# Performance work log

Measured on AMD Instinct MI355X. Metric: run time of the kernel, lower is better.

The kernel has to match this reference:

```python
import jax, jax.numpy as jnp
import numpy as np

VOCAB = 267735
CUTOFFS = [20000, 40000, 200000, VOCAB]  # self.cutoffs (incl. vocab)
SHORTLIST = 20000
N_CLUSTERS = 3


def setup_inputs() -> dict:
    key = jax.random.key(0)
    ks = jax.random.split(key, 16)
    s = 0.02  # init scale as in reset_parameters / linear_weight_init
    return {
        "x": jax.random.normal(ks[0], (1024, 1024), jnp.float32),
        "target": jax.random.randint(ks[1], (1024,), 0, VOCAB, jnp.int64),
        "W0": s * jax.random.normal(ks[2], (20000, 1024), jnp.float32),
        "b0": jnp.zeros((20000,), jnp.float32),
        "W1": s * jax.random.normal(ks[3], (20000, 256), jnp.float32),
        "b1": jnp.zeros((20000,), jnp.float32),
        "W2": s * jax.random.normal(ks[4], (160000, 64), jnp.float32),
        "b2": jnp.zeros((160000,), jnp.float32),
        "W3": s * jax.random.normal(ks[5], (67735, 16), jnp.float32),
        "b3": jnp.zeros((67735,), jnp.float32),
        "cluster_weight": s * jax.random.normal(ks[6], (3, 1024), jnp.float32),
        "cluster_bias": jnp.zeros((3,), jnp.float32),
        "P0": s * jax.random.normal(ks[7], (1024, 1024), jnp.float32),
        "P1": s * jax.random.normal(ks[8], (1024, 256), jnp.float32),
        "P2": s * jax.random.normal(ks[9], (1024, 64), jnp.float32),
        "P3": s * jax.random.normal(ks[10], (1024, 16), jnp.float32),
    }


def _logits(x, P, W, b):
    # F.linear(hidden, proj.t()) == x @ proj ; then F.linear(proj_hid, W, b)
    return (x @ P) @ W.T + b


def reference(x, target, W0, b0, W1, b1, W2, b2, W3, b3,
              cluster_weight, cluster_bias, P0, P1, P2, P3):
    N = x.shape[0]
    # head: shortlist + cluster logits
    head_w = jnp.concatenate([W0, cluster_weight], axis=0)  # [20003, 1024]
    head_b = jnp.concatenate([b0, cluster_bias], axis=0)
    head_logp = jax.nn.log_softmax(_logits(x, P0, head_w, head_b), axis=-1)

    # remap targets falling in tail clusters to their cluster token in the head
    # cluster idx -> head index SHORTLIST + N_CLUSTERS - 1 - idx
    head_idx = target
    for idx in range(N_CLUSTERS):
        l, r = CUTOFFS[idx], CUTOFFS[idx + 1]
        in_c = (target >= l) & (target < r)
        head_idx = jnp.where(in_c, SHORTLIST + N_CLUSTERS - 1 - idx, head_idx)

    nll = -jnp.take_along_axis(head_logp, head_idx[:, None], axis=1)[:, 0]

    # tail clusters: dense masked cross-entropy (same math as gather/scatter
    # version: each token contributes only its own cluster's CE)
    tails = [(W1, b1, P1), (W2, b2, P2), (W3, b3, P3)]
    for idx, (W, b, P) in enumerate(tails):
        l, r = CUTOFFS[idx], CUTOFFS[idx + 1]
        mask = (target >= l) & (target < r)
        t = jnp.clip(target - l, 0, r - l - 1)
        logp = jax.nn.log_softmax(_logits(x, P, W, b), axis=-1)  # [N, r-l]
        ce = -jnp.take_along_axis(logp, t[:, None], axis=1)[:, 0]
        nll = nll + jnp.where(mask, ce, jnp.zeros_like(ce))
    return nll
```

## Files before the change

### kernel.cpp

```cpp
#include <hip/hip_runtime.h>
#include <hip/hip_bf16.h>
#include <math.h>


typedef __attribute__((ext_vector_type(4))) float f32x4;
typedef __attribute__((ext_vector_type(8))) short bf16x8;
typedef __attribute__((ext_vector_type(8))) unsigned short ushort8;

#define NEG_INF (-INFINITY)

static __device__ __forceinline__ unsigned short f2b(float f) {
  unsigned u = __builtin_bit_cast(unsigned, f);
  u += 0x7fffu + ((u >> 16) & 1u);
  return (unsigned short)(u >> 16);
}
static __device__ __forceinline__ f32x4 zero4() { f32x4 z = {0.f,0.f,0.f,0.f}; return z; }
static __device__ __forceinline__ ushort8 zero8() { ushort8 z = {0,0,0,0,0,0,0,0}; return z; }

__global__ __launch_bounds__(256, 3)
void gemm_lse(const unsigned short* __restrict__ A, const float* __restrict__ B,
              const float* __restrict__ bias, int V, int K, int T,
              float* __restrict__ parts)
{
  __shared__ unsigned short As[128 * 40];
  __shared__ unsigned short Bs[128 * 40];
  __shared__ float red[2][128];

  const int t = threadIdx.x;
  const int rowBase = blockIdx.y * 128;
  const int strip = blockIdx.x;
  const int KS = (K + 31) >> 5;

  const int ar = t >> 1, ak = (t & 1) << 4;
  const int br = t >> 1, bk = (t & 1) << 4;
  const size_t arow = (size_t)(rowBase + ar) * K;

  ushort8 aSb[2]; f32x4 bS[4];
  auto LOADB = [&](int tile, int k0) {
    size_t row = (size_t)(strip * T + tile) * 128 + br;
    bool v = row < (size_t)V;
    const float* bp = B + row * (size_t)K;
    #pragma unroll
    for (int i = 0; i < 4; ++i) {
      int k = k0 + bk + i * 4;
      bS[i] = (v && (k + 4 <= K)) ? *(const f32x4*)(bp + k) : zero4();
    }
  };
  auto LOADA = [&](int k0) {
    #pragma unroll
    for (int i = 0; i < 2; ++i) {
      int k = k0 + ak + i * 8;
      aSb[i] = (k + 8 <= K) ? *(const ushort8*)(A + arow + k) : zero8();
    }
  };
  auto STORE = [&]() {
    *(ushort8*)&As[ar * 40 + ak]     = aSb[0];
    *(ushort8*)&As[ar * 40 + ak + 8] = aSb[1];
    ushort8 p0, p1;
    #pragma unroll
    for (int j = 0; j < 4; ++j) {
      p0[j] = f2b(bS[0][j]); p0[j + 4] = f2b(bS[1][j]);
      p1[j] = f2b(bS[2][j]); p1[j + 4] = f2b(bS[3][j]);
    }
    *(ushort8*)&Bs[br * 40 + bk]     = p0;
    *(ushort8*)&Bs[br * 40 + bk + 8] = p1;
  };

  const int lane = t & 63, w = t >> 6;
  const int wr = w >> 1, wc = w & 1;
  const int g = lane >> 4, fr = lane & 15;

  float S[4][4];
  #pragma unroll
  for (int m = 0; m < 4; ++m)
    #pragma unroll
    for (int r = 0; r < 4; ++r) S[m][r] = 0.f;
  f32x4 acc[4][4];
  #pragma unroll
  for (int m = 0; m < 4; ++m)
    #pragma unroll
    for (int n = 0; n < 4; ++n) acc[m][n] = zero4();

  float bcol[4];
  LOADB(0, 0); LOADA(0);
  int tile = 0, ks = 0;
  const int total = T * KS;
  for (int step = 0; step < total; ++step) {
    __syncthreads();
    STORE();
    __syncthreads();
    if (ks == 0) {
      #pragma unroll
      for (int n = 0; n < 4; ++n) {
        int col = (strip * T + tile) * 128 + wc * 64 + n * 16 + fr;
        bcol[n] = (col < V) ? bias[col] : NEG_INF;
      }
    }
    const bool last = (ks == KS - 1);
    int nt = tile, nk = ks + 1;
    if (nk == KS) { nk = 0; nt++; }
    if (nt < T) { LOADB(nt, nk * 32); LOADA(nk * 32); }
    bf16x8 af[4], bfr[4];
    #pragma unroll
    for (int m = 0; m < 4; ++m)
      af[m] = *(const bf16x8*)&As[(wr * 64 + m * 16 + fr) * 40 + g * 8];
    #pragma unroll
    for (int n = 0; n < 4; ++n)
      bfr[n] = *(const bf16x8*)&Bs[(wc * 64 + n * 16 + fr) * 40 + g * 8];
    #pragma unroll
    for (int m = 0; m < 4; ++m)
      #pragma unroll
      for (int n = 0; n < 4; ++n)
        acc[m][n] = __builtin_amdgcn_mfma_f32_16x16x32_bf16(af[m], bfr[n], acc[m][n], 0, 0, 0);
    if (last) {
      #pragma unroll
      for (int m = 0; m < 4; ++m)
        #pragma unroll
        for (int n = 0; n < 4; ++n)
          #pragma unroll
          for (int r = 0; r < 4; ++r)
            S[m][r] += __expf(acc[m][n][r] + bcol[n]);
      #pragma unroll
      for (int m = 0; m < 4; ++m)
        #pragma unroll
        for (int n = 0; n < 4; ++n) acc[m][n] = zero4();
    }
    tile = nt; ks = nk;
  }

  #pragma unroll
  for (int off = 1; off <= 8; off <<= 1)
    #pragma unroll
    for (int m = 0; m < 4; ++m)
      #pragma unroll
      for (int r = 0; r < 4; ++r) S[m][r] += __shfl_xor(S[m][r], off, 64);
  if (fr == 0) {
    #pragma unroll
    for (int m = 0; m < 4; ++m)
      #pragma unroll
      for (int r = 0; r < 4; ++r) red[wc][wr * 64 + m * 16 + g * 4 + r] = S[m][r];
  }
  __syncthreads();
  if (t < 128) parts[(size_t)strip * 1024 + rowBase + t] = red[0][t] + red[1][t];
}

__global__ __launch_bounds__(256, 3)
void gemm_proj(const float* __restrict__ A, const unsigned short* __restrict__ B,
               int V, int K,
               float* __restrict__ Cf, unsigned short* __restrict__ Cb)
{
  __shared__ unsigned short As[128 * 40];
  __shared__ unsigned short Bs[128 * 40];

  const int t = threadIdx.x;
  const int rowBase = blockIdx.y * 128;
  const int colBase = blockIdx.x * 128;

  const int ar = t >> 1, ak = (t & 1) << 4;
  const int br = t >> 1, bk = (t & 1) << 4;
  const bool bval = (colBase + br) < V;
  const size_t arow = (size_t)(rowBase + ar) * K;
  const size_t brow = (size_t)(colBase + br) * K;

  f32x4 aS[4]; ushort8 bSb[2];
  auto LOAD = [&](int k0) {
    #pragma unroll
    for (int i = 0; i < 4; ++i) aS[i] = *(const f32x4*)(A + arow + k0 + ak + i * 4);
    bSb[0] = bval ? *(const ushort8*)(B + brow + k0 + bk)     : zero8();
    bSb[1] = bval ? *(const ushort8*)(B + brow + k0 + bk + 8) : zero8();
  };
  auto STORE = [&]() {
    ushort8 p0, p1;
    #pragma unroll
    for (int j = 0; j < 4; ++j) {
      p0[j] = f2b(aS[0][j]); p0[j + 4] = f2b(aS[1][j]);
      p1[j] = f2b(aS[2][j]); p1[j + 4] = f2b(aS[3][j]);
    }
    *(ushort8*)&As[ar * 40 + ak]     = p0;
    *(ushort8*)&As[ar * 40 + ak + 8] = p1;
    *(ushort8*)&Bs[br * 40 + bk]     = bSb[0];
    *(ushort8*)&Bs[br * 40 + bk + 8] = bSb[1];
  };

  const int lane = t & 63, w = t >> 6;
  const int wr = w >> 1, wc = w & 1;
  const int g = lane >> 4, fr = lane & 15;

  f32x4 acc[4][4];
  #pragma unroll
  for (int m = 0; m < 4; ++m)
    #pragma unroll
    for (int n = 0; n < 4; ++n) acc[m][n] = zero4();

  LOAD(0);
  for (int k0 = 0; k0 < K; k0 += 32) {
    __syncthreads();
    STORE();
    __syncthreads();
    if (k0 + 32 < K) LOAD(k0 + 32);
    bf16x8 af[4], bfr[4];
    #pragma unroll
    for (int m = 0; m < 4; ++m)
      af[m] = *(const bf16x8*)&As[(wr * 64 + m * 16 + fr) * 40 + g * 8];
    #pragma unroll
    for (int n = 0; n < 4; ++n)
      bfr[n] = *(const bf16x8*)&Bs[(wc * 64 + n * 16 + fr) * 40 + g * 8];
    #pragma unroll
    for (int m = 0; m < 4; ++m)
      #pragma unroll
      for (int n = 0; n < 4; ++n)
        acc[m][n] = __builtin_amdgcn_mfma_f32_16x16x32_bf16(af[m], bfr[n], acc[m][n], 0, 0, 0);
  }

  #pragma unroll
  for (int m = 0; m < 4; ++m) {
    int row = rowBase + wr * 64 + m * 16 + g * 4;
    #pragma unroll
    for (int n = 0; n < 4; ++n) {
      int col = colBase + wc * 64 + n * 16 + fr;
      if (col < V) {
        #pragma unroll
        for (int r = 0; r < 4; ++r) {
          float v = acc[m][n][r];
          Cf[(size_t)(row + r) * V + col] = v;
          Cb[(size_t)(row + r) * V + col] = f2b(v);
        }
      }
    }
  }
}

__global__ void transpose_k(const float* __restrict__ P, unsigned short* __restrict__ PT, int N)
{
  __shared__ float tile[32][33];
  int tx = threadIdx.x, ty = threadIdx.y;
  int n0 = blockIdx.x * 32, k0 = blockIdx.y * 32;
  #pragma unroll
  for (int j = 0; j < 32; j += 8) {
    int n = n0 + tx;
    tile[ty + j][tx] = (n < N) ? P[(size_t)(k0 + ty + j) * N + n] : 0.f;
  }
  __syncthreads();
  #pragma unroll
  for (int j = 0; j < 32; j += 8) {
    int n = n0 + ty + j;
    if (n < N) PT[(size_t)n * 1024 + (k0 + tx)] = f2b(tile[tx][ty + j]);
  }
}

__global__ void cluster_logits_k(const float* __restrict__ H0,
                                 const float* __restrict__ CW,
                                 const float* __restrict__ cb,
                                 float* __restrict__ clog)
{
  int wid = (blockIdx.x * blockDim.x + threadIdx.x) >> 6;
  int lane = threadIdx.x & 63;
  if (wid >= 1024) return;
  float s0 = 0.f, s1 = 0.f, s2 = 0.f;
  for (int k = lane * 4; k < 1024; k += 256) {
    f32x4 h  = *(const f32x4*)&H0[(size_t)wid * 1024 + k];
    f32x4 w0 = *(const f32x4*)&CW[k];
    f32x4 w1 = *(const f32x4*)&CW[1024 + k];
    f32x4 w2 = *(const f32x4*)&CW[2048 + k];
    #pragma unroll
    for (int j = 0; j < 4; ++j) { s0 += h[j]*w0[j]; s1 += h[j]*w1[j]; s2 += h[j]*w2[j]; }
  }
  #pragma unroll
  for (int off = 1; off <= 32; off <<= 1) {
    s0 += __shfl_xor(s0, off, 64);
    s1 += __shfl_xor(s1, off, 64);
    s2 += __shfl_xor(s2, off, 64);
  }
  if (lane == 0) {
    clog[wid * 3 + 0] = s0 + cb[0];
    clog[wid * 3 + 1] = s1 + cb[1];
    clog[wid * 3 + 2] = s2 + cb[2];
  }
}

__global__ void head_target_k(const float* __restrict__ H0,
                              const float* __restrict__ W0,
                              const float* __restrict__ b0,
                              const float* __restrict__ clog,
                              const int* __restrict__ target,
                              float* __restrict__ headT)
{
  int wid = (blockIdx.x * blockDim.x + threadIdx.x) >> 6;
  int lane = threadIdx.x & 63;
  if (wid >= 1024) return;
  int tg = target[wid];
  if (tg < 20000) {
    const float* wrow = W0 + (size_t)tg * 1024;
    float s = 0.f;
    for (int k = lane * 4; k < 1024; k += 256) {
      f32x4 h = *(const f32x4*)&H0[(size_t)wid * 1024 + k];
      f32x4 v = *(const f32x4*)&wrow[k];
      #pragma unroll
      for (int j = 0; j < 4; ++j) s += h[j] * v[j];
    }
    #pragma unroll
    for (int off = 1; off <= 32; off <<= 1) s += __shfl_xor(s, off, 64);
    if (lane == 0) headT[wid] = s + b0[tg];
  } else if (lane == 0) {
    int idx = (tg < 40000) ? 0 : (tg < 200000) ? 1 : 2;
    headT[wid] = clog[wid * 3 + (2 - idx)];
  }
}

__global__ void tail_target_k(const float* __restrict__ H1, const float* __restrict__ H2,
                              const float* __restrict__ H3,
                              const float* __restrict__ W1, const float* __restrict__ b1,
                              const float* __restrict__ W2, const float* __restrict__ b2,
                              const float* __restrict__ W3, const float* __restrict__ b3,
                              const int* __restrict__ target, float* __restrict__ tailT)
{
  int wid = (blockIdx.x * blockDim.x + threadIdx.x) >> 6;
  int lane = threadIdx.x & 63;
  if (wid >= 1024) return;
  int tg = target[wid];
  if (tg < 20000) { if (lane == 0) tailT[wid] = 0.f; return; }
  const float *H, *W, *bb; int Kc, l;
  if (tg < 40000)       { H = H1; W = W1; bb = b1; Kc = 256; l = 20000; }
  else if (tg < 200000) { H = H2; W = W2; bb = b2; Kc = 64;  l = 40000; }
  else                  { H = H3; W = W3; bb = b3; Kc = 16;  l = 200000; }
  int tt = tg - l;
  float s = 0.f;
  for (int k = lane * 4; k < Kc; k += 256) {
    f32x4 h = *(const f32x4*)&H[(size_t)wid * Kc + k];
    f32x4 v = *(const f32x4*)&W[(size_t)tt * Kc + k];
    #pragma unroll
    for (int j = 0; j < 4; ++j) s += h[j] * v[j];
  }
  #pragma unroll
  for (int off = 1; off <= 32; off <<= 1) s += __shfl_xor(s, off, 64);
  if (lane == 0) tailT[wid] = s + bb[tt];
}

__global__ void finalize_all(const float* __restrict__ parts,
                             const float* __restrict__ clog,
                             const float* __restrict__ headT,
                             const float* __restrict__ tailT,
                             const int* __restrict__ target,
                             float* __restrict__ out)
{
  int wid = (blockIdx.x * blockDim.x + threadIdx.x) >> 6;
  int lane = threadIdx.x & 63;
  if (wid >= 1024) return;
  float s1 = 0.f;
  for (int i = lane; i < 157; i += 64) s1 += parts[(size_t)i * 1024 + wid];
  if (lane < 3) s1 += __expf(clog[wid * 3 + lane]);
  int tg = target[wid];
  float s2 = 0.f;
  if (tg >= 20000) {
    const float* pT; int ns;
    if (tg < 40000)       { pT = parts + (size_t)157 * 1024; ns = 157; }
    else if (tg < 200000) { pT = parts + (size_t)314 * 1024; ns = 625; }
    else                  { pT = parts + (size_t)939 * 1024; ns = 265; }
    for (int i = lane; i < ns; i += 64) s2 += pT[(size_t)i * 1024 + wid];
  }
  #pragma unroll
  for (int off = 1; off <= 32; off <<= 1) {
    s1 += __shfl_xor(s1, off, 64);
    s2 += __shfl_xor(s2, off, 64);
  }
  if (lane == 0) {
    float nll = logf(s1) - headT[wid];
    if (tg >= 20000) nll += logf(s2) - tailT[wid];
    out[wid] = nll;
  }
}

extern "C" void kernel_launch(void* const* d_in, const int* in_sizes, int n_in,
                              void* d_out, int out_size, void* d_ws, size_t ws_size,
                              hipStream_t stream)
{
  const float* x   = (const float*)d_in[0];
  const int*   tgt = (const int*)d_in[1];
  const float* W0  = (const float*)d_in[2];
  const float* b0  = (const float*)d_in[3];
  const float* W1  = (const float*)d_in[4];
  const float* b1  = (const float*)d_in[5];
  const float* W2  = (const float*)d_in[6];
  const float* b2  = (const float*)d_in[7];
  const float* W3  = (const float*)d_in[8];
  const float* b3  = (const float*)d_in[9];
  const float* CW  = (const float*)d_in[10];
  const float* cb  = (const float*)d_in[11];
  const float* P0  = (const float*)d_in[12];
  const float* P1  = (const float*)d_in[13];
  const float* P2  = (const float*)d_in[14];
  const float* P3  = (const float*)d_in[15];
  float* out = (float*)d_out;

  char* ws = (char*)d_ws;
  size_t off = 0;
  auto alloc = [&](size_t bytes) -> void* {
    void* p = ws + off;
    off = (off + bytes + 255) & ~(size_t)255;
    return p;
  };
  unsigned short* PT0 = (unsigned short*)alloc((size_t)1024 * 1024 * 2);
  unsigned short* PT1 = (unsigned short*)alloc((size_t)256 * 1024 * 2);
  unsigned short* PT2 = (unsigned short*)alloc((size_t)64 * 1024 * 2);
  unsigned short* PT3 = (unsigned short*)alloc((size_t)16 * 1024 * 2);
  float* H0f = (float*)alloc((size_t)1024 * 1024 * 4);
  float* H1f = (float*)alloc((size_t)1024 * 256 * 4);
  float* H2f = (float*)alloc((size_t)1024 * 64 * 4);
  float* H3f = (float*)alloc((size_t)1024 * 16 * 4);
  unsigned short* H0b = (unsigned short*)alloc((size_t)1024 * 1024 * 2);
  unsigned short* H1b = (unsigned short*)alloc((size_t)1024 * 256 * 2);
  unsigned short* H2b = (unsigned short*)alloc((size_t)1024 * 64 * 2);
  unsigned short* H3b = (unsigned short*)alloc((size_t)1024 * 16 * 2);
  float* parts = (float*)alloc((size_t)1204 * 1024 * 4);
  float* clog  = (float*)alloc((size_t)1024 * 3 * 4);
  float* headT = (float*)alloc((size_t)1024 * 4);
  float* tailT = (float*)alloc((size_t)1024 * 4);

  float* pHead = parts;
  float* pT1   = parts + (size_t)157 * 1024;
  float* pT2   = parts + (size_t)314 * 1024;
  float* pT3   = parts + (size_t)939 * 1024;

  dim3 tb(32, 8);
  transpose_k<<<dim3(32, 32), tb, 0, stream>>>(P0, PT0, 1024);
  transpose_k<<<dim3(8, 32),  tb, 0, stream>>>(P1, PT1, 256);
  transpose_k<<<dim3(2, 32),  tb, 0, stream>>>(P2, PT2, 64);
  transpose_k<<<dim3(1, 32),  tb, 0, stream>>>(P3, PT3, 16);

  gemm_proj<<<dim3(8, 8), 256, 0, stream>>>(x, PT0, 1024, 1024, H0f, H0b);
  gemm_proj<<<dim3(2, 8), 256, 0, stream>>>(x, PT1, 256,  1024, H1f, H1b);
  gemm_proj<<<dim3(1, 8), 256, 0, stream>>>(x, PT2, 64,   1024, H2f, H2b);
  gemm_proj<<<dim3(1, 8), 256, 0, stream>>>(x, PT3, 16,   1024, H3f, H3b);

  cluster_logits_k<<<256, 256, 0, stream>>>(H0f, CW, cb, clog);
  head_target_k<<<256, 256, 0, stream>>>(H0f, W0, b0, clog, tgt, headT);
  tail_target_k<<<256, 256, 0, stream>>>(H1f, H2f, H3f, W1, b1, W2, b2, W3, b3, tgt, tailT);

  gemm_lse<<<dim3(157, 8), 256, 0, stream>>>(H0b, W0, b0, 20000,  1024, 1, pHead);
  gemm_lse<<<dim3(157, 8), 256, 0, stream>>>(H1b, W1, b1, 20000,  256,  1, pT1);
  gemm_lse<<<dim3(625, 8), 256, 0, stream>>>(H2b, W2, b2, 160000, 64,   2, pT2);
  gemm_lse<<<dim3(265, 8), 256, 0, stream>>>(H3b, W3, b3, 67735,  16,   2, pT3);

  finalize_all<<<256, 256, 0, stream>>>(parts, clog, headT, tailT, tgt, out);
}
```

Measured before the change: 559.3 us.

## Give each LSE block one column tile and swizzle the grid for cache locality

gemm_lse no longer loops over T column tiles per block; each block handles exactly one 128-column tile. A 1D grid is remapped so that groups of 8 consecutive blocks share a column group across row blocks, which should improve L2 reuse of the fp32 weight rows. The tail kernels now launch more blocks, which needs a larger partial-sum buffer and matching finalize offsets. Launch bounds are raised to 4 waves per SIMD for occupancy, at the cost of tighter register limits and possible spills.

Result: slower. 623.6 us (+11.5%).

```diff
diff --git a/kernel.cpp b/kernel.cpp
--- a/kernel.cpp
+++ b/kernel.cpp
@@ -17,40 +17,44 @@
 static __device__ __forceinline__ f32x4 zero4() { f32x4 z = {0.f,0.f,0.f,0.f}; return z; }
 static __device__ __forceinline__ ushort8 zero8() { ushort8 z = {0,0,0,0,0,0,0,0}; return z; }
 
-__global__ __launch_bounds__(256, 3)
+__global__ __launch_bounds__(256, 4)
 void gemm_lse(const unsigned short* __restrict__ A, const float* __restrict__ B,
-              const float* __restrict__ bias, int V, int K, int T,
+              const float* __restrict__ bias, int V, int K, int Ns, int q,
               float* __restrict__ parts)
 {
   __shared__ unsigned short As[128 * 40];
   __shared__ unsigned short Bs[128 * 40];
   __shared__ float red[2][128];
 
+  const int l = blockIdx.x;
+  const int c = l & 7, j = l >> 3;
+  const int s = c + 8 * (j % q);
+  const int rb = j / q;
+  if (s >= Ns) return;
+  const int rowBase = rb * 128;
+  const int colBase = s * 128;
+  const int KS = (K + 31) >> 5;
+
   const int t = threadIdx.x;
-  const int rowBase = blockIdx.y * 128;
-  const int strip = blockIdx.x;
-  const int KS = (K + 31) >> 5;
-
   const int ar = t >> 1, ak = (t & 1) << 4;
   const int br = t >> 1, bk = (t & 1) << 4;
   const size_t arow = (size_t)(rowBase + ar) * K;
+  const bool bv = (colBase + br) < V;
+  const float* bp = B + (size_t)(colBase + br) * K;
 
   ushort8 aSb[2]; f32x4 bS[4];
-  auto LOADB = [&](int tile, int k0) {
-    size_t row = (size_t)(strip * T + tile) * 128 + br;
-    bool v = row < (size_t)V;
-    const float* bp = B + row * (size_t)K;
-    #pragma unroll
-    for (int i = 0; i < 4; ++i) {
-      int k = k0 + bk + i * 4;
-      bS[i] = (v && (k + 4 <= K)) ? *(const f32x4*)(bp + k) : zero4();
-    }
-  };
   auto LOADA = [&](int k0) {
     #pragma unroll
     for (int i = 0; i < 2; ++i) {
       int k = k0 + ak + i * 8;
       aSb[i] = (k + 8 <= K) ? *(const ushort8*)(A + arow + k) : zero8();
+    }
+  };
+  auto LOADB = [&](int k0) {
+    #pragma unroll
+    for (int i = 0; i < 4; ++i) {
+      int k = k0 + bk + i * 4;
+      bS[i] = (bv && (k + 4 <= K)) ? *(const f32x4*)(bp + k) : zero4();
     }
   };
   auto STORE = [&]() {
@@ -58,9 +62,9 @@
     *(ushort8*)&As[ar * 40 + ak + 8] = aSb[1];
     ushort8 p0, p1;
     #pragma unroll
-    for (int j = 0; j < 4; ++j) {
-      p0[j] = f2b(bS[0][j]); p0[j + 4] = f2b(bS[1][j]);
-      p1[j] = f2b(bS[2][j]); p1[j + 4] = f2b(bS[3][j]);
+    for (int jj = 0; jj < 4; ++jj) {
+      p0[jj] = f2b(bS[0][jj]); p0[jj + 4] = f2b(bS[1][jj]);
+      p1[jj] = f2b(bS[2][jj]); p1[jj + 4] = f2b(bS[3][jj]);
     }
     *(ushort8*)&Bs[br * 40 + bk]     = p0;
     *(ushort8*)&Bs[br * 40 + bk + 8] = p1;
@@ -70,36 +74,18 @@
   const int wr = w >> 1, wc = w & 1;
   const int g = lane >> 4, fr = lane & 15;
 
-  float S[4][4];
+  f32x4 acc[4][4];
   #pragma unroll
   for (int m = 0; m < 4; ++m)
     #pragma unroll
-    for (int r = 0; r < 4; ++r) S[m][r] = 0.f;
-  f32x4 acc[4][4];
-  #pragma unroll
-  for (int m = 0; m < 4; ++m)
-    #pragma unroll
     for (int n = 0; n < 4; ++n) acc[m][n] = zero4();
 
-  float bcol[4];
-  LOADB(0, 0); LOADA(0);
-  int tile = 0, ks = 0;
-  const int total = T * KS;
-  for (int step = 0; step < total; ++step) {
+  LOADA(0); LOADB(0);
+  for (int ks = 0; ks < KS; ++ks) {
     __syncthreads();
     STORE();
     __syncthreads();
-    if (ks == 0) {
-      #pragma unroll
-      for (int n = 0; n < 4; ++n) {
-        int col = (strip * T + tile) * 128 + wc * 64 + n * 16 + fr;
-        bcol[n] = (col < V) ? bias[col] : NEG_INF;
-      }
-    }
-    const bool last = (ks == KS - 1);
-    int nt = tile, nk = ks + 1;
-    if (nk == KS) { nk = 0; nt++; }
-    if (nt < T) { LOADB(nt, nk * 32); LOADA(nk * 32); }
+    if (ks + 1 < KS) { LOADA(ks * 32 + 32); LOADB(ks * 32 + 32); }
     bf16x8 af[4], bfr[4];
     #pragma unroll
     for (int m = 0; m < 4; ++m)
@@ -112,21 +98,24 @@
       #pragma unroll
       for (int n = 0; n < 4; ++n)
         acc[m][n] = __builtin_amdgcn_mfma_f32_16x16x32_bf16(af[m], bfr[n], acc[m][n], 0, 0, 0);
-    if (last) {
-      #pragma unroll
-      for (int m = 0; m < 4; ++m)
-        #pragma unroll
-        for (int n = 0; n < 4; ++n)
-          #pragma unroll
-          for (int r = 0; r < 4; ++r)
-            S[m][r] += __expf(acc[m][n][r] + bcol[n]);
-      #pragma unroll
-      for (int m = 0; m < 4; ++m)
-        #pragma unroll
-        for (int n = 0; n < 4; ++n) acc[m][n] = zero4();
-    }
-    tile = nt; ks = nk;
-  }
+  }
+
+  float bcol[4];
+  #pragma unroll
+  for (int n = 0; n < 4; ++n) {
+    int col = colBase + wc * 64 + n * 16 + fr;
+    bcol[n] = (col < V) ? bias[col] : NEG_INF;
+  }
+  float S[4][4];
+  #pragma unroll
+  for (int m = 0; m < 4; ++m)
+    #pragma unroll
+    for (int r = 0; r < 4; ++r) {
+      float acc_s = 0.f;
+      #pragma unroll
+      for (int n = 0; n < 4; ++n) acc_s += __expf(acc[m][n][r] + bcol[n]);
+      S[m][r] = acc_s;
+    }
 
   #pragma unroll
   for (int off = 1; off <= 8; off <<= 1)
@@ -141,10 +130,10 @@
       for (int r = 0; r < 4; ++r) red[wc][wr * 64 + m * 16 + g * 4 + r] = S[m][r];
   }
   __syncthreads();
-  if (t < 128) parts[(size_t)strip * 1024 + rowBase + t] = red[0][t] + red[1][t];
-}
-
-__global__ __launch_bounds__(256, 3)
+  if (t < 128) parts[(size_t)s * 1024 + rowBase + t] = red[0][t] + red[1][t];
+}
+
+__global__ __launch_bounds__(256, 4)
 void gemm_proj(const float* __restrict__ A, const unsigned short* __restrict__ B,
                int V, int K,
                float* __restrict__ Cf, unsigned short* __restrict__ Cb)
@@ -172,9 +161,9 @@
   auto STORE = [&]() {
     ushort8 p0, p1;
     #pragma unroll
-    for (int j = 0; j < 4; ++j) {
-      p0[j] = f2b(aS[0][j]); p0[j + 4] = f2b(aS[1][j]);
-      p1[j] = f2b(aS[2][j]); p1[j + 4] = f2b(aS[3][j]);
+    for (int jj = 0; jj < 4; ++jj) {
+      p0[jj] = f2b(aS[0][jj]); p0[jj + 4] = f2b(aS[1][jj]);
+      p1[jj] = f2b(aS[2][jj]); p1[jj + 4] = f2b(aS[3][jj]);
     }
     *(ushort8*)&As[ar * 40 + ak]     = p0;
     *(ushort8*)&As[ar * 40 + ak + 8] = p1;
@@ -353,9 +342,9 @@
   float s2 = 0.f;
   if (tg >= 20000) {
     const float* pT; int ns;
-    if (tg < 40000)       { pT = parts + (size_t)157 * 1024; ns = 157; }
-    else if (tg < 200000) { pT = parts + (size_t)314 * 1024; ns = 625; }
-    else                  { pT = parts + (size_t)939 * 1024; ns = 265; }
+    if (tg < 40000)       { pT = parts + (size_t)157  * 1024; ns = 157;  }
+    else if (tg < 200000) { pT = parts + (size_t)314  * 1024; ns = 1250; }
+    else                  { pT = parts + (size_t)1564 * 1024; ns = 530;  }
     for (int i = lane; i < ns; i += 64) s2 += pT[(size_t)i * 1024 + wid];
   }
   #pragma unroll
@@ -411,15 +400,15 @@
   unsigned short* H1b = (unsigned short*)alloc((size_t)1024 * 256 * 2);
   unsigned short* H2b = (unsigned short*)alloc((size_t)1024 * 64 * 2);
   unsigned short* H3b = (unsigned short*)alloc((size_t)1024 * 16 * 2);
-  float* parts = (float*)alloc((size_t)1204 * 1024 * 4);
+  float* parts = (float*)alloc((size_t)2094 * 1024 * 4);
   float* clog  = (float*)alloc((size_t)1024 * 3 * 4);
   float* headT = (float*)alloc((size_t)1024 * 4);
   float* tailT = (float*)alloc((size_t)1024 * 4);
 
   float* pHead = parts;
-  float* pT1   = parts + (size_t)157 * 1024;
-  float* pT2   = parts + (size_t)314 * 1024;
-  float* pT3   = parts + (size_t)939 * 1024;
+  float* pT1   = parts + (size_t)157  * 1024;
+  float* pT2   = parts + (size_t)314  * 1024;
+  float* pT3   = parts + (size_t)1564 * 1024;
 
   dim3 tb(32, 8);
   transpose_k<<<dim3(32, 32), tb, 0, stream>>>(P0, PT0, 1024);
@@ -436,10 +425,10 @@
   head_target_k<<<256, 256, 0, stream>>>(H0f, W0, b0, clog, tgt, headT);
   tail_target_k<<<256, 256, 0, stream>>>(H1f, H2f, H3f, W1, b1, W2, b2, W3, b3, tgt, tailT);
 
-  gemm_lse<<<dim3(157, 8), 256, 0, stream>>>(H0b, W0, b0, 20000,  1024, 1, pHead);
-  gemm_lse<<<dim3(157, 8), 256, 0, stream>>>(H1b, W1, b1, 20000,  256,  1, pT1);
-  gemm_lse<<<dim3(625, 8), 256, 0, stream>>>(H2b, W2, b2, 160000, 64,   2, pT2);
-  gemm_lse<<<dim3(265, 8), 256, 0, stream>>>(H3b, W3, b3, 67735,  16,   2, pT3);
+  gemm_lse<<<20 * 64,  256, 0, stream>>>(H0b, W0, b0, 20000,  1024, 157,  20,  pHead);
+  gemm_lse<<<20 * 64,  256, 0, stream>>>(H1b, W1, b1, 20000,  256,  157,  20,  pT1);
+  gemm_lse<<<157 * 64, 256, 0, stream>>>(H2b, W2, b2, 160000, 64,   1250, 157, pT2);
+  gemm_lse<<<67 * 64,  256, 0, stream>>>(H3b, W3, b3, 67735,  16,   530,  67,  pT3);
 
   finalize_all<<<256, 256, 0, stream>>>(parts, clog, headT, tailT, tgt, out);
 }
```
